# Optimization experiments

Hardware: AMD Instinct MI355X
Metric: run time of the kernel (lower is better)

Reference implementation:

```python
import jax, jax.numpy as jnp
import numpy as np

B, P, N, D = 32, 100, 1000, 128
SQRT_D = 11.313708498984761
CLIP = 10.0


def setup_inputs() -> dict:
    key = jax.random.key(0)
    ks = jax.random.split(key, 8)
    s = 1.0 / np.sqrt(D)  # keep k ~ N(0,1) so exp(k) is stable
    return {
        "encoded_nodes": jax.random.normal(ks[0], (B, N, D), jnp.float32),
        "encoded_q1": jax.random.normal(ks[1], (B, P, D), jnp.float32),
        "encoded_last_node": jax.random.normal(ks[2], (B, P, D), jnp.float32),
        "cur_dist": jax.random.uniform(ks[3], (B, P, N), jnp.float32),
        "ninf_mask": jnp.zeros((B, P, N), jnp.float32),
        "log_scale": jnp.ones((1,), jnp.float32),
        "Wq_first": jax.random.normal(ks[4], (D, D), jnp.float32) * s,
        "Wq_last": jax.random.normal(ks[5], (D, D), jnp.float32) * s,
        "Wk": jax.random.normal(ks[6], (D, D), jnp.float32) * s,
        "Wv": jax.random.normal(ks[7], (D, D), jnp.float32) * s,
        "dist_alpha_1": jnp.ones((1,), jnp.float32),
        "AFT_dist_alpha_1": jnp.ones((1,), jnp.float32),
    }


def reference(encoded_nodes, encoded_q1, encoded_last_node, cur_dist, ninf_mask,
              log_scale, Wq_first, Wq_last, Wk, Wv, dist_alpha_1, AFT_dist_alpha_1):
    # set_kv / set_q1 (torch Linear: x @ W.T)
    k = jnp.einsum('bnd,ed->bne', encoded_nodes, Wk)          # [B,N,D]
    v = jnp.einsum('bnd,ed->bne', encoded_nodes, Wv)          # [B,N,D]
    q_first = jnp.einsum('bpd,ed->bpe', encoded_q1, Wq_first) # [B,P,D]
    q_last = jnp.einsum('bpd,ed->bpe', encoded_last_node, Wq_last)
    q = q_first + q_last

    cur_dist_out = -cur_dist                                   # [B,P,N]
    bias_scale = log_scale * AFT_dist_alpha_1 * cur_dist_out + ninf_mask
    ebias = jnp.exp(bias_scale)                                # [B,P,N]
    ek = jnp.exp(k)                                            # [B,N,D]
    num = jnp.einsum('bpn,bnd->bpd', ebias, ek * v)
    den = jnp.einsum('bpn,bnd->bpd', ebias, ek)
    aft_out = jax.nn.sigmoid(q) * (num / den)                  # [B,P,D]

    score = jnp.einsum('bpd,bnd->bpn', aft_out, encoded_nodes) / SQRT_D
    score = score + log_scale * dist_alpha_1 * cur_dist_out
    score = CLIP * jnp.tanh(score) + ninf_mask
    return jax.nn.softmax(score, axis=2)
```

## Files before the change

### kernel.cpp

```cpp
#include <hip/hip_runtime.h>
#include <hip/hip_bf16.h>
#include <math.h>

#define B 32
#define P 100
#define N 1000
#define D 128

constexpr float SQRT_D_INV = 1.0f / 11.313708498984761f;
constexpr float CLIPV = 10.0f;

__device__ __forceinline__ void fma4(float4& a, float s, const float4& b) {
    a.x = fmaf(s, b.x, a.x);
    a.y = fmaf(s, b.y, a.y);
    a.z = fmaf(s, b.z, a.z);
    a.w = fmaf(s, b.w, a.w);
}

#define TT 64
__global__ __launch_bounds__(256) void prep_kernel(
        const float* __restrict__ nodes,
        const float* __restrict__ Wk,  const float* __restrict__ Wv,
        const float* __restrict__ Wqf, const float* __restrict__ Wql,
        float* __restrict__ wkT,  float* __restrict__ wvT,
        float* __restrict__ wqfT, float* __restrict__ wqlT,
        float* __restrict__ nodesT) {
    const int t = threadIdx.x;
    if (blockIdx.x < D) {
        const int e = blockIdx.x;
        const int d = t & 127;
        if ((t >> 7) == 0) {
            wkT[e * D + d] = Wk[d * D + e];
            wvT[e * D + d] = Wv[d * D + e];
        } else {
            wqfT[e * D + d] = Wqf[d * D + e];
            wqlT[e * D + d] = Wql[d * D + e];
        }
        return;
    }
    __shared__ float sh[TT][D + 1];
    const int blk = blockIdx.x - D;
    const int ntiles = (N + TT - 1) / TT;
    const int b  = blk / ntiles;
    const int n0 = (blk % ntiles) * TT;
    const int rows = min(TT, N - n0);

    const float4* src = (const float4*)(nodes + ((long)b * N + n0) * D);
    for (int i = t; i < rows * (D / 4); i += 256) {
        int r = i >> 5, c = i & 31;
        float4 v = src[(long)r * (D / 4) + c];
        sh[r][c * 4 + 0] = v.x; sh[r][c * 4 + 1] = v.y;
        sh[r][c * 4 + 2] = v.z; sh[r][c * 4 + 3] = v.w;
    }
    __syncthreads();

    const int nl = t & 63;
    const int eg = t >> 6;
    if (nl < rows) {
        #pragma unroll
        for (int k = 0; k < 32; ++k) {
            int e = eg * 32 + k;
            nodesT[((long)b * D + e) * N + n0 + nl] = sh[nl][e];
        }
    }
}

#define R1 32
__global__ __launch_bounds__(256) void kv_kernel(
        const float* __restrict__ nodes,
        const float* __restrict__ wkT,
        const float* __restrict__ wvT,
        float* __restrict__ ek,
        float* __restrict__ ekv) {
    __shared__ float sh[R1][D];
    const int t = threadIdx.x;
    const int dq = t & 31;
    const int rl = t >> 5;
    const long row0 = (long)blockIdx.x * R1;

    const float4* src = (const float4*)(nodes + row0 * D);
    float4* dst = (float4*)(&sh[0][0]);
    #pragma unroll
    for (int i = 0; i < (R1 * D / 4) / 256; ++i)
        dst[t + i * 256] = src[t + i * 256];
    __syncthreads();

    float4 ka[4], va[4];
    #pragma unroll
    for (int rr = 0; rr < 4; ++rr) {
        ka[rr] = make_float4(0.f, 0.f, 0.f, 0.f);
        va[rr] = make_float4(0.f, 0.f, 0.f, 0.f);
    }

    const float* wkp = wkT + dq * 4;
    const float* wvp = wvT + dq * 4;

    float4 cwk[4], cwv[4];
    #pragma unroll
    for (int ee = 0; ee < 4; ++ee) {
        cwk[ee] = *(const float4*)(wkp + ee * D);
        cwv[ee] = *(const float4*)(wvp + ee * D);
    }

    for (int e0 = 0; e0 < D; e0 += 4) {
        float4 nwk[4], nwv[4];
        if (e0 + 4 < D) {
            #pragma unroll
            for (int ee = 0; ee < 4; ++ee) {
                nwk[ee] = *(const float4*)(wkp + (e0 + 4 + ee) * D);
                nwv[ee] = *(const float4*)(wvp + (e0 + 4 + ee) * D);
            }
        }
        #pragma unroll
        for (int rr = 0; rr < 4; ++rr) {
            float4 s4 = *(const float4*)(&sh[rl * 4 + rr][e0]);
            fma4(ka[rr], s4.x, cwk[0]); fma4(ka[rr], s4.y, cwk[1]);
            fma4(ka[rr], s4.z, cwk[2]); fma4(ka[rr], s4.w, cwk[3]);
            fma4(va[rr], s4.x, cwv[0]); fma4(va[rr], s4.y, cwv[1]);
            fma4(va[rr], s4.z, cwv[2]); fma4(va[rr], s4.w, cwv[3]);
        }
        #pragma unroll
        for (int ee = 0; ee < 4; ++ee) { cwk[ee] = nwk[ee]; cwv[ee] = nwv[ee]; }
    }

    #pragma unroll
    for (int rr = 0; rr < 4; ++rr) {
        long row = row0 + rl * 4 + rr;
        float4 e4;
        e4.x = __expf(ka[rr].x); e4.y = __expf(ka[rr].y);
        e4.z = __expf(ka[rr].z); e4.w = __expf(ka[rr].w);
        float4 ev;
        ev.x = e4.x * va[rr].x; ev.y = e4.y * va[rr].y;
        ev.z = e4.z * va[rr].z; ev.w = e4.w * va[rr].w;
        *(float4*)(ek + row * D + dq * 4) = e4;
        *(float4*)(ekv + row * D + dq * 4) = ev;
    }
}

#define R2 16
__global__ __launch_bounds__(256) void q_kernel(
        const float* __restrict__ q1,
        const float* __restrict__ qlast,
        const float* __restrict__ wqfT,
        const float* __restrict__ wqlT,
        float* __restrict__ qsig) {
    __shared__ float sh1[R2][D];
    __shared__ float sh2[R2][D];
    const int t = threadIdx.x;
    const int dq = t & 31;
    const int rl = t >> 5;
    const long row0 = (long)blockIdx.x * R2;

    const float4* s1 = (const float4*)(q1 + row0 * D);
    const float4* s2 = (const float4*)(qlast + row0 * D);
    float4* d1 = (float4*)(&sh1[0][0]);
    float4* d2 = (float4*)(&sh2[0][0]);
    #pragma unroll
    for (int i = 0; i < (R2 * D / 4) / 256; ++i) {
        d1[t + i * 256] = s1[t + i * 256];
        d2[t + i * 256] = s2[t + i * 256];
    }
    __syncthreads();

    float4 acc[2];
    acc[0] = make_float4(0.f, 0.f, 0.f, 0.f);
    acc[1] = make_float4(0.f, 0.f, 0.f, 0.f);

    const float* wfp = wqfT + dq * 4;
    const float* wlp = wqlT + dq * 4;

    float4 cwf[4], cwl[4];
    #pragma unroll
    for (int ee = 0; ee < 4; ++ee) {
        cwf[ee] = *(const float4*)(wfp + ee * D);
        cwl[ee] = *(const float4*)(wlp + ee * D);
    }

    for (int e0 = 0; e0 < D; e0 += 4) {
        float4 nwf[4], nwl[4];
        if (e0 + 4 < D) {
            #pragma unroll
            for (int ee = 0; ee < 4; ++ee) {
                nwf[ee] = *(const float4*)(wfp + (e0 + 4 + ee) * D);
                nwl[ee] = *(const float4*)(wlp + (e0 + 4 + ee) * D);
            }
        }
        #pragma unroll
        for (int rr = 0; rr < 2; ++rr) {
            float4 a4 = *(const float4*)(&sh1[rl * 2 + rr][e0]);
            float4 b4 = *(const float4*)(&sh2[rl * 2 + rr][e0]);
            fma4(acc[rr], a4.x, cwf[0]); fma4(acc[rr], a4.y, cwf[1]);
            fma4(acc[rr], a4.z, cwf[2]); fma4(acc[rr], a4.w, cwf[3]);
            fma4(acc[rr], b4.x, cwl[0]); fma4(acc[rr], b4.y, cwl[1]);
            fma4(acc[rr], b4.z, cwl[2]); fma4(acc[rr], b4.w, cwl[3]);
        }
        #pragma unroll
        for (int ee = 0; ee < 4; ++ee) { cwf[ee] = nwf[ee]; cwl[ee] = nwl[ee]; }
    }

    #pragma unroll
    for (int rr = 0; rr < 2; ++rr) {
        long row = row0 + rl * 2 + rr;
        float4 s;
        s.x = 1.0f / (1.0f + __expf(-acc[rr].x));
        s.y = 1.0f / (1.0f + __expf(-acc[rr].y));
        s.z = 1.0f / (1.0f + __expf(-acc[rr].z));
        s.w = 1.0f / (1.0f + __expf(-acc[rr].w));
        *(float4*)(qsig + row * D + dq * 4) = s;
    }
}

#define PT 20
#define TS 32
__global__ __launch_bounds__(128) void aft_part_kernel(
        const float* __restrict__ cur_dist,
        const float* __restrict__ ninf,
        const float* __restrict__ ek,
        const float* __restrict__ ekv,
        const float* __restrict__ log_scale,
        const float* __restrict__ aft_alpha,
        float* __restrict__ pnum,
        float* __restrict__ pden,
        int NC, int L) {
    __shared__ float eb[2][TS][33];
    const int t = threadIdx.x;
    const int dq = t & 31;
    const int pl = t >> 5;
    const int pl5 = pl * 5;
    const int b    = blockIdx.x % B;
    const int rest = blockIdx.x / B;
    const int c    = rest % NC;
    const int pt   = rest / NC;
    const int p0 = pt * PT;
    const int n_begin = c * L;
    const int n_end = min(N, n_begin + L);
    const float lsA = log_scale[0] * aft_alpha[0];

    float4 num[5], den[5];
    #pragma unroll
    for (int i = 0; i < 5; ++i) {
        num[i] = make_float4(0.f, 0.f, 0.f, 0.f);
        den[i] = make_float4(0.f, 0.f, 0.f, 0.f);
    }

    float rv[5];
    int n0 = n_begin;
    int ts = min(TS, n_end - n0);

    #pragma unroll
    for (int k = 0; k < 5; ++k) {
        int s = t + k * 128;
        int pp = s >> 5, nl = s & 31;
        rv[k] = 0.f;
        if (nl < ts) {
            long idx = ((long)b * P + p0 + pp) * N + (n0 + nl);
            rv[k] = fmaf(-lsA, cur_dist[idx], ninf[idx]);
        }
    }

    int buf = 0;
    while (n0 < n_end) {
        #pragma unroll
        for (int k = 0; k < 5; ++k) {
            int s = t + k * 128;
            int pp = s >> 5, nl = s & 31;
            if (nl < ts) eb[buf][nl][pp] = __expf(rv[k]);
        }
        __syncthreads();

        const int n0n = n0 + ts;
        const int tsn = min(TS, n_end - n0n);
        if (n0n < n_end) {
            #pragma unroll
            for (int k = 0; k < 5; ++k) {
                int s = t + k * 128;
                int pp = s >> 5, nl = s & 31;
                rv[k] = 0.f;
                if (nl < tsn) {
                    long idx = ((long)b * P + p0 + pp) * N + (n0n + nl);
                    rv[k] = fmaf(-lsA, cur_dist[idx], ninf[idx]);
                }
            }
        }

        const float* ekb = ek  + ((long)b * N + n0) * D + dq * 4;
        const float* evb = ekv + ((long)b * N + n0) * D + dq * 4;
        #pragma unroll 4
        for (int j = 0; j < ts; ++j) {
            float4 ekq = *(const float4*)(ekb + (long)j * D);
            float4 evq = *(const float4*)(evb + (long)j * D);
            float e0 = eb[buf][j][pl5 + 0];
            float e1 = eb[buf][j][pl5 + 1];
            float e2 = eb[buf][j][pl5 + 2];
            float e3 = eb[buf][j][pl5 + 3];
            float e4 = eb[buf][j][pl5 + 4];
            fma4(num[0], e0, evq); fma4(den[0], e0, ekq);
            fma4(num[1], e1, evq); fma4(den[1], e1, ekq);
            fma4(num[2], e2, evq); fma4(den[2], e2, ekq);
            fma4(num[3], e3, evq); fma4(den[3], e3, ekq);
            fma4(num[4], e4, evq); fma4(den[4], e4, ekq);
        }
        buf ^= 1;
        n0 = n0n;
        ts = tsn;
    }

    #pragma unroll
    for (int r = 0; r < 5; ++r) {
        int p = p0 + pl5 + r;
        long o = (((long)c * B + b) * P + p) * D + dq * 4;
        *(float4*)(pnum + o) = num[r];
        *(float4*)(pden + o) = den[r];
    }
}

__global__ __launch_bounds__(256) void aft_reduce_kernel(
        const float* __restrict__ pnum,
        const float* __restrict__ pden,
        const float* __restrict__ qsig,
        float* __restrict__ aft,
        int NC) {
    const long i = (long)blockIdx.x * 256 + threadIdx.x;
    const long BPD = (long)B * P * D;
    float n = 0.f, d = 0.f;
    for (int c = 0; c < NC; ++c) {
        n += pnum[(long)c * BPD + i];
        d += pden[(long)c * BPD + i];
    }
    aft[i] = qsig[i] * n / d;
}

#define PT2 10
#define SC 4
__global__ __launch_bounds__(128) void score_part_kernel(
        const float* __restrict__ aft,
        const float* __restrict__ nodesT,
        const float* __restrict__ cur_dist,
        const float* __restrict__ ninf,
        const float* __restrict__ log_scale,
        const float* __restrict__ dist_alpha,
        float* __restrict__ out,
        float* __restrict__ sums) {
    __shared__ float sa[PT2][D];
    __shared__ float red[2][PT2];
    const int t = threadIdx.x;
    const int wid = t >> 6;
    const int b    = blockIdx.x % B;
    const int rest = blockIdx.x / B;
    const int c    = rest % SC;
    const int pt   = rest / SC;
    const int p0 = pt * PT2;
    const float lsA = log_scale[0] * dist_alpha[0];

    for (int i = t; i < PT2 * D; i += 128) {
        sa[i >> 7][i & 127] = aft[((long)b * P + p0) * D + i];
    }
    __syncthreads();

    const int n0 = c * 256 + t * 2;
    const bool act = (n0 < N);
    const int ncl = act ? n0 : 0;
    const float* ntb = nodesT + (long)b * D * N;

    float2 acc[PT2];
    #pragma unroll
    for (int i = 0; i < PT2; ++i) acc[i] = make_float2(0.f, 0.f);

    float2 cx[4];
    #pragma unroll
    for (int ee = 0; ee < 4; ++ee)
        cx[ee] = *(const float2*)(ntb + (long)ee * N + ncl);

    for (int e0 = 0; e0 < D; e0 += 4) {
        float2 nx[4];
        if (e0 + 4 < D) {
            #pragma unroll
            for (int ee = 0; ee < 4; ++ee)
                nx[ee] = *(const float2*)(ntb + (long)(e0 + 4 + ee) * N + ncl);
        }
        #pragma unroll
        for (int i = 0; i < PT2; ++i) {
            float4 a4 = *(const float4*)(&sa[i][e0]);
            acc[i].x = fmaf(cx[0].x, a4.x, acc[i].x);
            acc[i].x = fmaf(cx[1].x, a4.y, acc[i].x);
            acc[i].x = fmaf(cx[2].x, a4.z, acc[i].x);
            acc[i].x = fmaf(cx[3].x, a4.w, acc[i].x);
            acc[i].y = fmaf(cx[0].y, a4.x, acc[i].y);
            acc[i].y = fmaf(cx[1].y, a4.y, acc[i].y);
            acc[i].y = fmaf(cx[2].y, a4.z, acc[i].y);
            acc[i].y = fmaf(cx[3].y, a4.w, acc[i].y);
        }
        #pragma unroll
        for (int ee = 0; ee < 4; ++ee) cx[ee] = nx[ee];
    }

    #pragma unroll
    for (int i = 0; i < PT2; ++i) {
        float2 ev = make_float2(0.f, 0.f);
        if (act) {
            long idx = ((long)b * P + p0 + i) * N + n0;
            float2 cd = *(const float2*)(cur_dist + idx);
            float2 nf = *(const float2*)(ninf + idx);
            float sx = fmaf(acc[i].x, SQRT_D_INV, -lsA * cd.x);
            float sy = fmaf(acc[i].y, SQRT_D_INV, -lsA * cd.y);
            float ax = fabsf(sx), ay = fabsf(sy);
            float rx = 1.f - 2.f / (__expf(2.f * ax) + 1.f);
            float ry = 1.f - 2.f / (__expf(2.f * ay) + 1.f);
            float scx = CLIPV * copysignf(rx, sx) + nf.x;
            float scy = CLIPV * copysignf(ry, sy) + nf.y;
            ev.x = __expf(scx);
            ev.y = __expf(scy);
            *(float2*)(out + idx) = ev;
        }
        float s = ev.x + ev.y;
        #pragma unroll
        for (int o = 1; o < 64; o <<= 1) s += __shfl_xor(s, o, 64);
        if ((t & 63) == 0) red[wid][i] = s;
    }
    __syncthreads();
    if (t < PT2) {
        atomicAdd(&sums[b * P + p0 + t], red[0][t] + red[1][t]);
    }
}

__global__ __launch_bounds__(256) void normalize_kernel(
        float* __restrict__ out, const float* __restrict__ sums) {
    const int row = blockIdx.x;
    const int t = threadIdx.x;
    const float inv = 1.0f / sums[row];
    float4* r = (float4*)(out + (long)row * N);
    if (t < N / 4) {
        float4 v = r[t];
        v.x *= inv; v.y *= inv; v.z *= inv; v.w *= inv;
        r[t] = v;
    }
}

extern "C" void kernel_launch(void* const* d_in, const int* in_sizes, int n_in,
                              void* d_out, int out_size, void* d_ws, size_t ws_size,
                              hipStream_t stream) {
    const float* nodes      = (const float*)d_in[0];
    const float* q1         = (const float*)d_in[1];
    const float* qlast      = (const float*)d_in[2];
    const float* cur_dist   = (const float*)d_in[3];
    const float* ninf       = (const float*)d_in[4];
    const float* log_scale  = (const float*)d_in[5];
    const float* Wqf        = (const float*)d_in[6];
    const float* Wql        = (const float*)d_in[7];
    const float* Wk         = (const float*)d_in[8];
    const float* Wv         = (const float*)d_in[9];
    const float* dist_alpha = (const float*)d_in[10];
    const float* aft_alpha  = (const float*)d_in[11];
    float* out = (float*)d_out;

    const long BND = (long)B * N * D;
    const long BPD = (long)B * P * D;
    const long W2  = (long)D * D;

    float* ws     = (float*)d_ws;
    float* ek     = ws;
    float* ekv    = ek + BND;
    float* qsig   = ekv + BND;
    float* aft    = qsig + BPD;
    float* wkT    = aft + BPD;
    float* wvT    = wkT + W2;
    float* wqfT   = wvT + W2;
    float* wqlT   = wqfT + W2;
    float* nodesT = wqlT + W2;
    float* sums   = nodesT + BND;
    float* pnum   = sums + (long)B * P;

    long avail = (long)(ws_size / 4) - (3 * BND + 2 * BPD + 4 * W2 + (long)B * P);
    int NC = (int)(avail / (2 * BPD));
    if (NC < 1) NC = 1;
    if (NC > 12) NC = 12;
    int L = (N + NC - 1) / NC;
    NC = (N + L - 1) / L;
    float* pden = pnum + (long)NC * BPD;

    hipMemsetAsync(sums, 0, (size_t)B * P * sizeof(float), stream);
    prep_kernel<<<D + B * ((N + TT - 1) / TT), 256, 0, stream>>>(
        nodes, Wk, Wv, Wqf, Wql, wkT, wvT, wqfT, wqlT, nodesT);
    kv_kernel<<<(B * N) / R1, 256, 0, stream>>>(nodes, wkT, wvT, ek, ekv);
    q_kernel<<<(B * P) / R2, 256, 0, stream>>>(q1, qlast, wqfT, wqlT, qsig);
    aft_part_kernel<<<B * (P / PT) * NC, 128, 0, stream>>>(
        cur_dist, ninf, ek, ekv, log_scale, aft_alpha, pnum, pden, NC, L);
    aft_reduce_kernel<<<(int)(BPD / 256), 256, 0, stream>>>(pnum, pden, qsig, aft, NC);
    score_part_kernel<<<B * SC * (P / PT2), 128, 0, stream>>>(
        aft, nodesT, cur_dist, ninf, log_scale, dist_alpha, out, sums);
    normalize_kernel<<<B * P, 256, 0, stream>>>(out, sums);
}
```

Before: 248.3 us.

## Stage ek/ekv tiles into LDS via async global_load_lds and vectorize AFT reduce

The AFT partial kernel now copies ek and ekv tiles into double-buffered shared memory using the async global-to-LDS load builtin. The inner loop then reads from LDS instead of doing per-thread global float4 loads, and the tile size shrinks to 16 rows with the eb indexing reworked to match. The chunk length L is rounded up to a multiple of 4, presumably so odd tile sizes are avoided in the pairwise copy. The reduce kernel is vectorized to float4 and unrolled over chunk pairs. Risks: there is no explicit wait on the async LDS loads before the single barrier, so correctness depends on how the compiler inserts vmcnt waits, and the smaller tiles mean more barriers.

```diff
diff --git a/kernel.cpp b/kernel.cpp
--- a/kernel.cpp
+++ b/kernel.cpp
@@ -211,7 +211,12 @@
 }
 
 #define PT 20
-#define TS 32
+#define TS3 16
+
+#define GLDS(gsrc, ldst) __builtin_amdgcn_global_load_lds( \
+    (const __attribute__((address_space(1))) void*)(gsrc), \
+    (__attribute__((address_space(3))) void*)(ldst), 16, 0, 0)
+
 __global__ __launch_bounds__(128) void aft_part_kernel(
         const float* __restrict__ cur_dist,
         const float* __restrict__ ninf,
@@ -222,9 +227,13 @@
         float* __restrict__ pnum,
         float* __restrict__ pden,
         int NC, int L) {
-    __shared__ float eb[2][TS][33];
+    __shared__ __align__(16) float ekL[2][TS3 * D];
+    __shared__ __align__(16) float evL[2][TS3 * D];
+    __shared__ __align__(16) float eb[2][TS3][33];
     const int t = threadIdx.x;
-    const int dq = t & 31;
+    const int lane = t & 63;
+    const int wid = t >> 6;
+    const int dq4 = (t & 31) * 4;
     const int pl = t >> 5;
     const int pl5 = pl * 5;
     const int b    = blockIdx.x % B;
@@ -243,64 +252,81 @@
         den[i] = make_float4(0.f, 0.f, 0.f, 0.f);
     }
 
-    float rv[5];
+    const float* ekc = ek  + (long)b * N * D;
+    const float* evc = ekv + (long)b * N * D;
+
     int n0 = n_begin;
-    int ts = min(TS, n_end - n0);
-
-    #pragma unroll
-    for (int k = 0; k < 5; ++k) {
+    int ts = min(TS3, n_end - n0);
+
+    {
+        const float* gk = ekc + (long)n0 * D;
+        const float* gv = evc + (long)n0 * D;
+        for (int i = wid; i < ts / 2; i += 2) {
+            GLDS(gk + i * 256 + lane * 4, &ekL[0][i * 256]);
+            GLDS(gv + i * 256 + lane * 4, &evL[0][i * 256]);
+        }
+    }
+    float rv[3];
+    #pragma unroll
+    for (int k = 0; k < 3; ++k) {
         int s = t + k * 128;
-        int pp = s >> 5, nl = s & 31;
+        int pp = s >> 4, nl = s & 15;
         rv[k] = 0.f;
-        if (nl < ts) {
+        if (s < PT * TS3 && nl < ts) {
             long idx = ((long)b * P + p0 + pp) * N + (n0 + nl);
             rv[k] = fmaf(-lsA, cur_dist[idx], ninf[idx]);
         }
     }
 
-    int buf = 0;
+    int cur = 0;
     while (n0 < n_end) {
         #pragma unroll
-        for (int k = 0; k < 5; ++k) {
+        for (int k = 0; k < 3; ++k) {
             int s = t + k * 128;
-            int pp = s >> 5, nl = s & 31;
-            if (nl < ts) eb[buf][nl][pp] = __expf(rv[k]);
+            int pp = s >> 4, nl = s & 15;
+            if (s < PT * TS3 && nl < ts) eb[cur][nl][pp] = __expf(rv[k]);
         }
         __syncthreads();
 
         const int n0n = n0 + ts;
-        const int tsn = min(TS, n_end - n0n);
+        const int tsn = min(TS3, n_end - n0n);
         if (n0n < n_end) {
+            const float* gk = ekc + (long)n0n * D;
+            const float* gv = evc + (long)n0n * D;
+            for (int i = wid; i < tsn / 2; i += 2) {
+                GLDS(gk + i * 256 + lane * 4, &ekL[cur ^ 1][i * 256]);
+                GLDS(gv + i * 256 + lane * 4, &evL[cur ^ 1][i * 256]);
+            }
             #pragma unroll
-            for (int k = 0; k < 5; ++k) {
+            for (int k = 0; k < 3; ++k) {
                 int s = t + k * 128;
-                int pp = s >> 5, nl = s & 31;
+                int pp = s >> 4, nl = s & 15;
                 rv[k] = 0.f;
-                if (nl < tsn) {
+                if (s < PT * TS3 && nl < tsn) {
                     long idx = ((long)b * P + p0 + pp) * N + (n0n + nl);
                     rv[k] = fmaf(-lsA, cur_dist[idx], ninf[idx]);
                 }
             }
         }
 
-        const float* ekb = ek  + ((long)b * N + n0) * D + dq * 4;
-        const float* evb = ekv + ((long)b * N + n0) * D + dq * 4;
+        const float* ekp = &ekL[cur][dq4];
+        const float* evp = &evL[cur][dq4];
         #pragma unroll 4
         for (int j = 0; j < ts; ++j) {
-            float4 ekq = *(const float4*)(ekb + (long)j * D);
-            float4 evq = *(const float4*)(evb + (long)j * D);
-            float e0 = eb[buf][j][pl5 + 0];
-            float e1 = eb[buf][j][pl5 + 1];
-            float e2 = eb[buf][j][pl5 + 2];
-            float e3 = eb[buf][j][pl5 + 3];
-            float e4 = eb[buf][j][pl5 + 4];
+            float4 ekq = *(const float4*)(ekp + j * D);
+            float4 evq = *(const float4*)(evp + j * D);
+            float e0 = eb[cur][j][pl5 + 0];
+            float e1 = eb[cur][j][pl5 + 1];
+            float e2 = eb[cur][j][pl5 + 2];
+            float e3 = eb[cur][j][pl5 + 3];
+            float e4 = eb[cur][j][pl5 + 4];
             fma4(num[0], e0, evq); fma4(den[0], e0, ekq);
             fma4(num[1], e1, evq); fma4(den[1], e1, ekq);
             fma4(num[2], e2, evq); fma4(den[2], e2, ekq);
             fma4(num[3], e3, evq); fma4(den[3], e3, ekq);
             fma4(num[4], e4, evq); fma4(den[4], e4, ekq);
         }
-        buf ^= 1;
+        cur ^= 1;
         n0 = n0n;
         ts = tsn;
     }
@@ -308,7 +334,7 @@
     #pragma unroll
     for (int r = 0; r < 5; ++r) {
         int p = p0 + pl5 + r;
-        long o = (((long)c * B + b) * P + p) * D + dq * 4;
+        long o = (((long)c * B + b) * P + p) * D + dq4;
         *(float4*)(pnum + o) = num[r];
         *(float4*)(pden + o) = den[r];
     }
@@ -320,14 +346,34 @@
         const float* __restrict__ qsig,
         float* __restrict__ aft,
         int NC) {
-    const long i = (long)blockIdx.x * 256 + threadIdx.x;
+    const long i = ((long)blockIdx.x * 256 + threadIdx.x) * 4;
     const long BPD = (long)B * P * D;
-    float n = 0.f, d = 0.f;
-    for (int c = 0; c < NC; ++c) {
-        n += pnum[(long)c * BPD + i];
-        d += pden[(long)c * BPD + i];
-    }
-    aft[i] = qsig[i] * n / d;
+    float4 n = make_float4(0.f, 0.f, 0.f, 0.f);
+    float4 d = make_float4(0.f, 0.f, 0.f, 0.f);
+    int c = 0;
+    for (; c + 2 <= NC; c += 2) {
+        float4 a0 = *(const float4*)(pnum + (long)c * BPD + i);
+        float4 a1 = *(const float4*)(pnum + (long)(c + 1) * BPD + i);
+        float4 b0 = *(const float4*)(pden + (long)c * BPD + i);
+        float4 b1 = *(const float4*)(pden + (long)(c + 1) * BPD + i);
+        n.x += a0.x + a1.x; n.y += a0.y + a1.y;
+        n.z += a0.z + a1.z; n.w += a0.w + a1.w;
+        d.x += b0.x + b1.x; d.y += b0.y + b1.y;
+        d.z += b0.z + b1.z; d.w += b0.w + b1.w;
+    }
+    if (c < NC) {
+        float4 a0 = *(const float4*)(pnum + (long)c * BPD + i);
+        float4 b0 = *(const float4*)(pden + (long)c * BPD + i);
+        n.x += a0.x; n.y += a0.y; n.z += a0.z; n.w += a0.w;
+        d.x += b0.x; d.y += b0.y; d.z += b0.z; d.w += b0.w;
+    }
+    float4 q = *(const float4*)(qsig + i);
+    float4 o;
+    o.x = q.x * n.x / d.x;
+    o.y = q.y * n.y / d.y;
+    o.z = q.z * n.z / d.z;
+    o.w = q.w * n.w / d.w;
+    *(float4*)(aft + i) = o;
 }
 
 #define PT2 10
@@ -474,7 +520,7 @@
     int NC = (int)(avail / (2 * BPD));
     if (NC < 1) NC = 1;
     if (NC > 12) NC = 12;
-    int L = (N + NC - 1) / NC;
+    int L = (((N + NC - 1) / NC) + 3) & ~3;
     NC = (N + L - 1) / L;
     float* pden = pnum + (long)NC * BPD;
 
@@ -485,7 +531,7 @@
     q_kernel<<<(B * P) / R2, 256, 0, stream>>>(q1, qlast, wqfT, wqlT, qsig);
     aft_part_kernel<<<B * (P / PT) * NC, 128, 0, stream>>>(
         cur_dist, ninf, ek, ekv, log_scale, aft_alpha, pnum, pden, NC, L);
-    aft_reduce_kernel<<<(int)(BPD / 256), 256, 0, stream>>>(pnum, pden, qsig, aft, NC);
+    aft_reduce_kernel<<<(int)(BPD / 1024), 256, 0, stream>>>(pnum, pden, qsig, aft, NC);
     score_part_kernel<<<B * SC * (P / PT2), 128, 0, stream>>>(
         aft, nodesT, cur_dist, ninf, log_scale, dist_alpha, out, sums);
     normalize_kernel<<<B * P, 256, 0, stream>>>(out, sums);
```

Measured after the change: 249.4 us. No clear change (+0.4%).
